# Performance work log

Hardware: AMD Instinct MI355X
Metric: run time of the kernel (lower is better)

## Reference

```python
import jax, jax.numpy as jnp
import numpy as np

EPS = 1e-5  # torch LayerNorm default


def _layer_norm(x, g, b):
    mu = jnp.mean(x, axis=-1, keepdims=True)
    var = jnp.mean(jnp.square(x - mu), axis=-1, keepdims=True)
    return (x - mu) * jax.lax.rsqrt(var + EPS) * g + b


def setup_inputs() -> dict:
    key = jax.random.key(0)
    ks = jax.random.split(key, 8)
    B, S, D = 4, 2048, 1024
    s = 1.0 / np.sqrt(D)
    return {
        "q": jax.random.normal(ks[0], (B, S, D), jnp.float32),
        "k": jax.random.normal(ks[1], (B, S, D), jnp.float32),
        "v": jax.random.normal(ks[2], (B, S, D), jnp.float32),
        "mask": jnp.ones((B, 1, S), jnp.int32),
        "Wq": jax.random.normal(ks[3], (D, D), jnp.float32) * s,
        "Wk": jax.random.normal(ks[4], (D, D), jnp.float32) * s,
        "Wv": jax.random.normal(ks[5], (D, D), jnp.float32) * s,
        "Wo": jax.random.normal(ks[6], (D, D), jnp.float32) * s,
        "ln_q_g": jnp.ones((D,), jnp.float32),
        "ln_q_b": jnp.zeros((D,), jnp.float32),
        "ln_k_g": jnp.ones((D,), jnp.float32),
        "ln_k_b": jnp.zeros((D,), jnp.float32),
        "ln_v_g": jnp.ones((D,), jnp.float32),
        "ln_v_b": jnp.zeros((D,), jnp.float32),
    }


def reference(q, k, v, mask, Wq, Wk, Wv, Wo,
              ln_q_g, ln_q_b, ln_k_g, ln_k_b, ln_v_g, ln_v_b):
    B, Lq, D = q.shape
    H = 16
    dk = D // H
    residual = q
    # pre-LN + bias-free projections
    qh = (_layer_norm(q, ln_q_g, ln_q_b) @ Wq).reshape(B, Lq, H, dk).transpose(0, 2, 1, 3)
    kh = (_layer_norm(k, ln_k_g, ln_k_b) @ Wk).reshape(B, -1, H, dk).transpose(0, 2, 1, 3)
    vh = (_layer_norm(v, ln_v_g, ln_v_b) @ Wv).reshape(B, -1, H, dk).transpose(0, 2, 1, 3)
    # scaled scores [B,H,Lq,Lk]
    scores = jnp.einsum('bhqd,bhkd->bhqk', qh, kh) / jnp.sqrt(jnp.float32(dk))
    pad = (mask == 0)[:, None, :, :]  # [B,1,*,Lk], True where masked
    scores = jnp.where(pad, -jnp.inf, scores)
    attn = jax.nn.softmax(scores, axis=-1)
    attn = jnp.where(pad, 0.0, attn)
    out = jnp.einsum('bhqk,bhkd->bhqd', attn, vh)
    out = out.transpose(0, 2, 1, 3).reshape(B, Lq, D)
    return out @ Wo + residual
```

## Files before the change

### kernel.cpp

```cpp
#include <hip/hip_runtime.h>
#include <stdint.h>

typedef __attribute__((ext_vector_type(8))) short short8;
typedef __attribute__((ext_vector_type(4))) float f32x4;
typedef __attribute__((ext_vector_type(4))) unsigned short us4;

#define B_ 4
#define S_ 2048
#define D_ 1024
#define H_ 16
#define DK_ 64

__device__ __forceinline__ unsigned short f2bf(float f) {
  union { float f; unsigned int u; } c; c.f = f;
  unsigned int r = (c.u + 0x7fffu + ((c.u >> 16) & 1u)) >> 16;
  return (unsigned short)r;
}

__device__ __forceinline__ unsigned int cvt_pk_bf16(float lo, float hi) {
  unsigned int r;
  asm("v_cvt_pk_bf16_f32 %0, %1, %2" : "=v"(r) : "v"(lo), "v"(hi));
  return r;
}

__device__ __forceinline__ float exp2_fast(float x) {
#if __has_builtin(__builtin_amdgcn_exp2f)
  return __builtin_amdgcn_exp2f(x);
#else
  float r; asm("v_exp_f32 %0, %1" : "=v"(r) : "v"(x)); return r;
#endif
}

__device__ __forceinline__ void glds16(const void* g, void* l) {
  __builtin_amdgcn_global_load_lds(
      (__attribute__((address_space(1))) void*)(uintptr_t)g,
      (__attribute__((address_space(3))) void*)l, 16, 0, 0);
}

__device__ __forceinline__ f32x4 mfma_bf16(short8 a, short8 b, f32x4 c) {
  return __builtin_amdgcn_mfma_f32_16x16x32_bf16(a, b, c, 0, 0, 0);
}

__global__ __launch_bounds__(256) void ln_bf16_3(const float* __restrict__ x0,
                                                 const float* __restrict__ x1,
                                                 const float* __restrict__ x2,
                                                 const float* __restrict__ g0,
                                                 const float* __restrict__ g1,
                                                 const float* __restrict__ g2,
                                                 const float* __restrict__ b0,
                                                 const float* __restrict__ b1,
                                                 const float* __restrict__ b2,
                                                 unsigned short* __restrict__ y0,
                                                 unsigned short* __restrict__ y1,
                                                 unsigned short* __restrict__ y2) {
  const int which = blockIdx.y;
  const float* x = which == 0 ? x0 : (which == 1 ? x1 : x2);
  const float* g = which == 0 ? g0 : (which == 1 ? g1 : g2);
  const float* bta = which == 0 ? b0 : (which == 1 ? b1 : b2);
  unsigned short* y = which == 0 ? y0 : (which == 1 ? y1 : y2);

  const int lane = threadIdx.x & 63, wid = threadIdx.x >> 6;
  const int row = blockIdx.x * 4 + wid;
  const float4* xr = (const float4*)(x + (size_t)row * D_);
  float4 v[4];
  float s1 = 0.f, s2 = 0.f;
#pragma unroll
  for (int i = 0; i < 4; ++i) {
    v[i] = xr[i * 64 + lane];
    s1 += v[i].x + v[i].y + v[i].z + v[i].w;
    s2 += v[i].x * v[i].x + v[i].y * v[i].y + v[i].z * v[i].z + v[i].w * v[i].w;
  }
#pragma unroll
  for (int m = 32; m; m >>= 1) { s1 += __shfl_xor(s1, m); s2 += __shfl_xor(s2, m); }
  const float mu = s1 * (1.f / D_);
  const float inv = rsqrtf(s2 * (1.f / D_) - mu * mu + 1e-5f);
  const float4* gp = (const float4*)g;
  const float4* bp = (const float4*)bta;
  us4* yr = (us4*)(y + (size_t)row * D_);
#pragma unroll
  for (int i = 0; i < 4; ++i) {
    float4 gv = gp[i * 64 + lane], bv = bp[i * 64 + lane];
    us4 o;
    o[0] = f2bf((v[i].x - mu) * inv * gv.x + bv.x);
    o[1] = f2bf((v[i].y - mu) * inv * gv.y + bv.y);
    o[2] = f2bf((v[i].z - mu) * inv * gv.z + bv.z);
    o[3] = f2bf((v[i].w - mu) * inv * gv.w + bv.w);
    yr[i * 64 + lane] = o;
  }
}

__global__ void wt_bf16_4(const float* __restrict__ W0, const float* __restrict__ W1,
                          const float* __restrict__ W2, const float* __restrict__ W3,
                          unsigned short* __restrict__ T0, unsigned short* __restrict__ T1,
                          unsigned short* __restrict__ T2, unsigned short* __restrict__ T3) {
  const int which = blockIdx.z;
  const float* W = which == 0 ? W0 : (which == 1 ? W1 : (which == 2 ? W2 : W3));
  unsigned short* Wt = which == 0 ? T0 : (which == 1 ? T1 : (which == 2 ? T2 : T3));
  __shared__ float t[32][33];
  const int n0 = blockIdx.x * 32, k0 = blockIdx.y * 32;
  const int tx = threadIdx.x, ty = threadIdx.y;
  for (int i = ty; i < 32; i += 8) t[i][tx] = W[(size_t)(k0 + i) * D_ + n0 + tx];
  __syncthreads();
  for (int i = ty; i < 32; i += 8)
    Wt[(size_t)(n0 + i) * D_ + k0 + tx] = f2bf(t[tx][i]);
}

template <int MODE>
__global__ __launch_bounds__(256, 2) void gemm_bt(const unsigned short* __restrict__ A,
                                                  const unsigned short* __restrict__ Bt,
                                                  void* __restrict__ outp, float scale,
                                                  const float* __restrict__ resid) {
  constexpr int K = D_;
  constexpr int NT = K / 64;
  __shared__ __attribute__((aligned(16))) unsigned short As[2][128][64];
  __shared__ __attribute__((aligned(16))) unsigned short Bs[2][128][64];
  const int tid = threadIdx.x;
  const int lane = tid & 63, wid = tid >> 6;
  const int lo16 = lane & 15, hi4 = lane >> 4;
  const int wr = wid >> 1, wc = wid & 1;
  const int gx = (int)gridDim.x;
  const int lid = (int)blockIdx.x + gx * (int)blockIdx.y;
  const int nwg = gx * (int)gridDim.y;
  const int swid = (lid & 7) * (nwg >> 3) + (lid >> 3);
  const int mbase = (swid / gx) * 128, nbase = (swid % gx) * 128;
  const int srow = lane >> 3, scol = (lane & 7) * 8;

  f32x4 acc[4][4] = {};

  auto stage = [&](int bufi, int kt) {
    const int kb = kt * 64;
#pragma unroll
    for (int c = 0; c < 4; ++c) {
      const int ch = wid * 4 + c;
      glds16(A + (size_t)(mbase + ch * 8 + srow) * K + kb + scol,
             (unsigned short*)&As[bufi][0][0] + ch * 512);
      glds16(Bt + (size_t)(nbase + ch * 8 + srow) * K + kb + scol,
             (unsigned short*)&Bs[bufi][0][0] + ch * 512);
    }
  };

  stage(0, 0);
  int cur = 0;

  for (int kt = 0; kt < NT; ++kt) {
    __syncthreads();
    if (kt + 1 < NT) stage(cur ^ 1, kt + 1);
    const unsigned short* Ap = &As[cur][0][0];
    const unsigned short* Bp = &Bs[cur][0][0];
    __builtin_amdgcn_s_setprio(1);
#pragma unroll
    for (int kk = 0; kk < 2; ++kk) {
      short8 af[4], bfr[4];
#pragma unroll
      for (int i = 0; i < 4; ++i)
        af[i] = *(const short8*)(Ap + (wr * 64 + i * 16 + lo16) * 64 + kk * 32 + hi4 * 8);
#pragma unroll
      for (int j = 0; j < 4; ++j)
        bfr[j] = *(const short8*)(Bp + (wc * 64 + j * 16 + lo16) * 64 + kk * 32 + hi4 * 8);
#pragma unroll
      for (int i = 0; i < 4; ++i)
#pragma unroll
        for (int j = 0; j < 4; ++j) acc[i][j] = mfma_bf16(af[i], bfr[j], acc[i][j]);
    }
    __builtin_amdgcn_s_setprio(0);
    cur ^= 1;
  }

  if (MODE == 0) {
    unsigned short* out = (unsigned short*)outp;
#pragma unroll
    for (int i = 0; i < 4; ++i) {
      const int row = mbase + wr * 64 + i * 16 + hi4 * 4;
      const int b = row >> 11, s = row & (S_ - 1);
#pragma unroll
      for (int j = 0; j < 4; ++j) {
        const int col = nbase + wc * 64 + j * 16 + lo16;
        const int h = col >> 6, d = col & 63;
        const size_t base = ((size_t)(b * H_ + h) * S_ + s) * DK_ + d;
#pragma unroll
        for (int r = 0; r < 4; ++r) out[base + (size_t)r * DK_] = f2bf(acc[i][j][r] * scale);
      }
    }
  } else if (MODE == 1) {
    float* out = (float*)outp;
#pragma unroll
    for (int i = 0; i < 4; ++i) {
      const int row = mbase + wr * 64 + i * 16 + hi4 * 4;
#pragma unroll
      for (int j = 0; j < 4; ++j) {
        const int col = nbase + wc * 64 + j * 16 + lo16;
        const size_t idx = (size_t)row * D_ + col;
#pragma unroll
        for (int r = 0; r < 4; ++r)
          out[idx + (size_t)r * D_] = acc[i][j][r] + resid[idx + (size_t)r * D_];
      }
    }
  } else {
    unsigned short* out = (unsigned short*)outp;
#pragma unroll
    for (int i = 0; i < 4; ++i) {
      const int row = mbase + wr * 64 + i * 16 + hi4 * 4;
      const int b = row >> 11, s0 = row & (S_ - 1);
#pragma unroll
      for (int j = 0; j < 4; ++j) {
        const int col = nbase + wc * 64 + j * 16 + lo16;
        const int h = col >> 6, d = col & 63;
        us4 w;
#pragma unroll
        for (int r = 0; r < 4; ++r) w[r] = f2bf(acc[i][j][r]);
        *(us4*)(out + ((size_t)(b * H_ + h) * DK_ + d) * S_ + s0) = w;
      }
    }
  }
}

__global__ __launch_bounds__(512, 2) void attn_k(const unsigned short* __restrict__ Qh,
                                                 const unsigned short* __restrict__ Kh,
                                                 const unsigned short* __restrict__ Vt,
                                                 const int* __restrict__ mask,
                                                 unsigned short* __restrict__ O) {
  __shared__ __attribute__((aligned(16))) unsigned short Ks[2][64][64];
  __shared__ __attribute__((aligned(16))) unsigned short Vs[2][64][64];
  __shared__ __attribute__((aligned(16))) unsigned short Ps[256][64];
  __shared__ unsigned short MskL[S_];
  __shared__ unsigned char TileOk[S_ / 64];
  const int tid = threadIdx.x, lane = tid & 63, wid = tid >> 6;
  const int lo16 = lane & 15, hi4 = lane >> 4;
  const int swz = (lo16 & 7) << 3;
  const int lid = (int)blockIdx.x + 8 * (int)blockIdx.y;
  const int swid = (lid & 7) * 64 + (lid >> 3);
  const int qb = swid & 7, bh = swid >> 3;
  const int b = bh >> 4, h = bh & 15;
  const unsigned short* Qb = Qh + (size_t)bh * S_ * DK_;
  const unsigned short* Kb = Kh + (size_t)bh * S_ * DK_;
  const unsigned short* Vb = Vt + (size_t)bh * DK_ * S_;
  const int* mb = mask + b * S_;
  const int srow = lane >> 3;
  const int scolx = ((lane & 7) ^ srow) * 8;

  for (int t = tid; t < S_; t += 512) MskL[t] = (unsigned short)(mb[t] != 0);
  __syncthreads();
  if (tid < S_ / 64) {
    int ok = 1;
    for (int j = 0; j < 64; ++j) ok &= (int)MskL[tid * 64 + j];
    TileOk[tid] = (unsigned char)ok;
  }

  short8 qf[2][2];
#pragma unroll
  for (int i = 0; i < 2; ++i)
#pragma unroll
    for (int kk = 0; kk < 2; ++kk)
      qf[i][kk] = *(const short8*)(Qb + (size_t)(qb * 256 + wid * 32 + i * 16 + lo16) * DK_ +
                                   kk * 32 + hi4 * 8);

  f32x4 o[2][4] = {};
  float lsum0 = 0.f, lsum1 = 0.f;

  auto stageKV = [&](int bufi, int kt) {
    glds16(Kb + (size_t)(kt * 64 + wid * 8 + srow) * DK_ + scolx,
           (unsigned short*)&Ks[bufi][0][0] + wid * 512);
    glds16(Vb + (size_t)(wid * 8 + srow) * S_ + kt * 64 + scolx,
           (unsigned short*)&Vs[bufi][0][0] + wid * 512);
  };

  stageKV(0, 0);
  int cur = 0;

  for (int kt = 0; kt < S_ / 64; ++kt) {
    __syncthreads();
    if (kt + 1 < S_ / 64) stageKV(cur ^ 1, kt + 1);

    const unsigned short* Kc = &Ks[cur][0][0];
    const int tok = (int)TileOk[kt];
#pragma unroll
    for (int i = 0; i < 2; ++i) {
      f32x4 p[4] = {};
      __builtin_amdgcn_s_setprio(1);
#pragma unroll
      for (int kk = 0; kk < 2; ++kk)
#pragma unroll
        for (int nf = 0; nf < 4; ++nf) {
          short8 kf = *(const short8*)(Kc + (nf * 16 + lo16) * 64 + ((kk * 32 + hi4 * 8) ^ swz));
          p[nf] = mfma_bf16(kf, qf[i][kk], p[nf]);
        }
      __builtin_amdgcn_s_setprio(0);
      if (!tok) {
#pragma unroll
        for (int nf = 0; nf < 4; ++nf) {
          const us4 mk = *(const us4*)&MskL[kt * 64 + nf * 16 + hi4 * 4];
#pragma unroll
          for (int r = 0; r < 4; ++r)
            if (!mk[r]) p[nf][r] = -1e30f;
        }
      }
      const int prow = wid * 32 + i * 16 + lo16;
      float ls = 0.f;
#pragma unroll
      for (int nf = 0; nf < 4; ++nf) {
        float e0 = exp2_fast(p[nf][0]);
        float e1 = exp2_fast(p[nf][1]);
        float e2 = exp2_fast(p[nf][2]);
        float e3 = exp2_fast(p[nf][3]);
        ls += (e0 + e1) + (e2 + e3);
        uint2 w;
        w.x = cvt_pk_bf16(e0, e1);
        w.y = cvt_pk_bf16(e2, e3);
        *(uint2*)&Ps[prow][(nf * 16 + hi4 * 4) ^ swz] = w;
      }
      if (i == 0) lsum0 += ls; else lsum1 += ls;
    }
    asm volatile("s_waitcnt lgkmcnt(0)" ::: "memory");
    __builtin_amdgcn_sched_barrier(0);
    const unsigned short* Vc = &Vs[cur][0][0];
    __builtin_amdgcn_s_setprio(1);
#pragma unroll
    for (int kk = 0; kk < 2; ++kk) {
      const int pc = (kk * 32 + hi4 * 8) ^ swz;
      short8 pa0 = *(const short8*)((const unsigned short*)Ps + (wid * 32 + 0 + lo16) * 64 + pc);
      short8 pa1 = *(const short8*)((const unsigned short*)Ps + (wid * 32 + 16 + lo16) * 64 + pc);
#pragma unroll
      for (int df = 0; df < 4; ++df) {
        short8 vf = *(const short8*)(Vc + (df * 16 + lo16) * 64 + pc);
        o[0][df] = mfma_bf16(pa0, vf, o[0][df]);
        o[1][df] = mfma_bf16(pa1, vf, o[1][df]);
      }
    }
    __builtin_amdgcn_s_setprio(0);
    cur ^= 1;
  }

  lsum0 += __shfl_xor(lsum0, 16); lsum0 += __shfl_xor(lsum0, 32);
  lsum1 += __shfl_xor(lsum1, 16); lsum1 += __shfl_xor(lsum1, 32);
#pragma unroll
  for (int i = 0; i < 2; ++i) {
#pragma unroll
    for (int r = 0; r < 4; ++r) {
      const int ql = hi4 * 4 + r;
      const float l = __shfl(i == 0 ? lsum0 : lsum1, ql);
      const float rl = l > 0.f ? 1.f / l : 0.f;
      const int srowg = qb * 256 + wid * 32 + i * 16 + ql;
      const size_t base = ((size_t)b * S_ + srowg) * D_ + h * 64;
#pragma unroll
      for (int df = 0; df < 4; ++df) O[base + df * 16 + lo16] = f2bf(o[i][df][r] * rl);
    }
  }
}

extern "C" void kernel_launch(void* const* d_in, const int* in_sizes, int n_in,
                              void* d_out, int out_size, void* d_ws, size_t ws_size,
                              hipStream_t stream) {
  const float* q = (const float*)d_in[0];
  const float* k = (const float*)d_in[1];
  const float* v = (const float*)d_in[2];
  const int* mask = (const int*)d_in[3];
  const float* Wq = (const float*)d_in[4];
  const float* Wk = (const float*)d_in[5];
  const float* Wv = (const float*)d_in[6];
  const float* Wo = (const float*)d_in[7];
  const float* lnqg = (const float*)d_in[8];
  const float* lnqb = (const float*)d_in[9];
  const float* lnkg = (const float*)d_in[10];
  const float* lnkb = (const float*)d_in[11];
  const float* lnvg = (const float*)d_in[12];
  const float* lnvb = (const float*)d_in[13];

  uint8_t* ws = (uint8_t*)d_ws;
  const size_t MB = 1024ull * 1024ull;
  unsigned short* Xq = (unsigned short*)(ws + 0 * MB);
  unsigned short* Xk = (unsigned short*)(ws + 16 * MB);
  unsigned short* Xv = (unsigned short*)(ws + 32 * MB);
  unsigned short* Wqt = (unsigned short*)(ws + 48 * MB);
  unsigned short* Wkt = (unsigned short*)(ws + 50 * MB);
  unsigned short* Wvt = (unsigned short*)(ws + 52 * MB);
  unsigned short* Wot = (unsigned short*)(ws + 54 * MB);
  unsigned short* Qh = (unsigned short*)(ws + 56 * MB);
  unsigned short* Kh = (unsigned short*)(ws + 72 * MB);
  unsigned short* Vtb = Xq;
  unsigned short* Ob = Xk;

  hipLaunchKernelGGL(wt_bf16_4, dim3(32, 32, 4), dim3(32, 8), 0, stream,
                     Wq, Wk, Wv, Wo, Wqt, Wkt, Wvt, Wot);

  hipLaunchKernelGGL(ln_bf16_3, dim3(2048, 3), dim3(256), 0, stream,
                     q, k, v, lnqg, lnkg, lnvg, lnqb, lnkb, lnvb, Xq, Xk, Xv);

  dim3 gg(D_ / 128, (B_ * S_) / 128);
  const float qscale = 0.125f * 1.4426950408889634f;
  hipLaunchKernelGGL(gemm_bt<0>, gg, dim3(256), 0, stream, Xq, Wqt, (void*)Qh, qscale, (const float*)nullptr);
  hipLaunchKernelGGL(gemm_bt<0>, gg, dim3(256), 0, stream, Xk, Wkt, (void*)Kh, 1.0f, (const float*)nullptr);
  hipLaunchKernelGGL(gemm_bt<2>, gg, dim3(256), 0, stream, Xv, Wvt, (void*)Vtb, 1.0f, (const float*)nullptr);

  hipLaunchKernelGGL(attn_k, dim3(S_ / 256, B_ * H_), dim3(512), 0, stream, Qh, Kh, Vtb, mask, Ob);

  hipLaunchKernelGGL(gemm_bt<1>, gg, dim3(256), 0, stream, Ob, Wot, d_out, 1.0f, q);
}
```

Before: 225.1 us.

## Batch QKV GEMMs into one launch and restructure attention tile loop

The three Q/K/V projection GEMMs become a single launch using blockIdx.z to pick inputs, outputs and epilogue. This removes two launches and lets the projection blocks fill the GPU together. The attention kernel now preloads K fragments before the QK MFMAs and pads the P buffer to 72 columns in place of the XOR swizzle. It also unrolls the KV loop by two with fixed buffer indices and drops the explicit lgkmcnt wait and sched barrier. The padding uses more shared memory, and dropping the wait relies on the compiler to order the LDS accesses correctly.

```diff
diff --git a/kernel.cpp b/kernel.cpp
--- a/kernel.cpp
+++ b/kernel.cpp
@@ -105,11 +105,113 @@
     Wt[(size_t)(n0 + i) * D_ + k0 + tx] = f2bf(t[tx][i]);
 }
 
-template <int MODE>
-__global__ __launch_bounds__(256, 2) void gemm_bt(const unsigned short* __restrict__ A,
-                                                  const unsigned short* __restrict__ Bt,
-                                                  void* __restrict__ outp, float scale,
-                                                  const float* __restrict__ resid) {
+__global__ __launch_bounds__(256, 2) void gemm_qkv(const unsigned short* __restrict__ Xq,
+                                                   const unsigned short* __restrict__ Xk,
+                                                   const unsigned short* __restrict__ Xv,
+                                                   const unsigned short* __restrict__ Wq,
+                                                   const unsigned short* __restrict__ Wk,
+                                                   const unsigned short* __restrict__ Wv,
+                                                   unsigned short* __restrict__ Qh,
+                                                   unsigned short* __restrict__ Kh,
+                                                   unsigned short* __restrict__ Vtb,
+                                                   float qscale) {
+  constexpr int K = D_;
+  constexpr int NT = K / 64;
+  __shared__ __attribute__((aligned(16))) unsigned short As[2][128][64];
+  __shared__ __attribute__((aligned(16))) unsigned short Bs[2][128][64];
+  const int z = blockIdx.z;
+  const unsigned short* A = z == 0 ? Xq : (z == 1 ? Xk : Xv);
+  const unsigned short* Bt = z == 0 ? Wq : (z == 1 ? Wk : Wv);
+  const int tid = threadIdx.x;
+  const int lane = tid & 63, wid = tid >> 6;
+  const int lo16 = lane & 15, hi4 = lane >> 4;
+  const int wr = wid >> 1, wc = wid & 1;
+  const int gx = (int)gridDim.x;
+  const int lid = (int)blockIdx.x + gx * (int)blockIdx.y;
+  const int nwg = gx * (int)gridDim.y;
+  const int swid = (lid & 7) * (nwg >> 3) + (lid >> 3);
+  const int mbase = (swid / gx) * 128, nbase = (swid % gx) * 128;
+  const int srow = lane >> 3, scol = (lane & 7) * 8;
+
+  f32x4 acc[4][4] = {};
+
+  auto stage = [&](int bufi, int kt) {
+    const int kb = kt * 64;
+#pragma unroll
+    for (int c = 0; c < 4; ++c) {
+      const int ch = wid * 4 + c;
+      glds16(A + (size_t)(mbase + ch * 8 + srow) * K + kb + scol,
+             (unsigned short*)&As[bufi][0][0] + ch * 512);
+      glds16(Bt + (size_t)(nbase + ch * 8 + srow) * K + kb + scol,
+             (unsigned short*)&Bs[bufi][0][0] + ch * 512);
+    }
+  };
+
+  stage(0, 0);
+  int cur = 0;
+
+  for (int kt = 0; kt < NT; ++kt) {
+    __syncthreads();
+    if (kt + 1 < NT) stage(cur ^ 1, kt + 1);
+    const unsigned short* Ap = &As[cur][0][0];
+    const unsigned short* Bp = &Bs[cur][0][0];
+    __builtin_amdgcn_s_setprio(1);
+#pragma unroll
+    for (int kk = 0; kk < 2; ++kk) {
+      short8 af[4], bfr[4];
+#pragma unroll
+      for (int i = 0; i < 4; ++i)
+        af[i] = *(const short8*)(Ap + (wr * 64 + i * 16 + lo16) * 64 + kk * 32 + hi4 * 8);
+#pragma unroll
+      for (int j = 0; j < 4; ++j)
+        bfr[j] = *(const short8*)(Bp + (wc * 64 + j * 16 + lo16) * 64 + kk * 32 + hi4 * 8);
+#pragma unroll
+      for (int i = 0; i < 4; ++i)
+#pragma unroll
+        for (int j = 0; j < 4; ++j) acc[i][j] = mfma_bf16(af[i], bfr[j], acc[i][j]);
+    }
+    __builtin_amdgcn_s_setprio(0);
+    cur ^= 1;
+  }
+
+  if (z < 2) {
+    unsigned short* out = z == 0 ? Qh : Kh;
+    const float scale = z == 0 ? qscale : 1.0f;
+#pragma unroll
+    for (int i = 0; i < 4; ++i) {
+      const int row = mbase + wr * 64 + i * 16 + hi4 * 4;
+      const int b = row >> 11, s = row & (S_ - 1);
+#pragma unroll
+      for (int j = 0; j < 4; ++j) {
+        const int col = nbase + wc * 64 + j * 16 + lo16;
+        const int h = col >> 6, d = col & 63;
+        const size_t base = ((size_t)(b * H_ + h) * S_ + s) * DK_ + d;
+#pragma unroll
+        for (int r = 0; r < 4; ++r) out[base + (size_t)r * DK_] = f2bf(acc[i][j][r] * scale);
+      }
+    }
+  } else {
+#pragma unroll
+    for (int i = 0; i < 4; ++i) {
+      const int row = mbase + wr * 64 + i * 16 + hi4 * 4;
+      const int b = row >> 11, s0 = row & (S_ - 1);
+#pragma unroll
+      for (int j = 0; j < 4; ++j) {
+        const int col = nbase + wc * 64 + j * 16 + lo16;
+        const int h = col >> 6, d = col & 63;
+        us4 w;
+#pragma unroll
+        for (int r = 0; r < 4; ++r) w[r] = f2bf(acc[i][j][r]);
+        *(us4*)(Vtb + ((size_t)(b * H_ + h) * DK_ + d) * S_ + s0) = w;
+      }
+    }
+  }
+}
+
+__global__ __launch_bounds__(256, 2) void gemm_out(const unsigned short* __restrict__ A,
+                                                   const unsigned short* __restrict__ Bt,
+                                                   float* __restrict__ out,
+                                                   const float* __restrict__ resid) {
   constexpr int K = D_;
   constexpr int NT = K / 64;
   __shared__ __attribute__((aligned(16))) unsigned short As[2][128][64];
@@ -166,50 +268,16 @@
     cur ^= 1;
   }
 
-  if (MODE == 0) {
-    unsigned short* out = (unsigned short*)outp;
-#pragma unroll
-    for (int i = 0; i < 4; ++i) {
-      const int row = mbase + wr * 64 + i * 16 + hi4 * 4;
-      const int b = row >> 11, s = row & (S_ - 1);
-#pragma unroll
-      for (int j = 0; j < 4; ++j) {
-        const int col = nbase + wc * 64 + j * 16 + lo16;
-        const int h = col >> 6, d = col & 63;
-        const size_t base = ((size_t)(b * H_ + h) * S_ + s) * DK_ + d;
-#pragma unroll
-        for (int r = 0; r < 4; ++r) out[base + (size_t)r * DK_] = f2bf(acc[i][j][r] * scale);
-      }
-    }
-  } else if (MODE == 1) {
-    float* out = (float*)outp;
-#pragma unroll
-    for (int i = 0; i < 4; ++i) {
-      const int row = mbase + wr * 64 + i * 16 + hi4 * 4;
-#pragma unroll
-      for (int j = 0; j < 4; ++j) {
-        const int col = nbase + wc * 64 + j * 16 + lo16;
-        const size_t idx = (size_t)row * D_ + col;
-#pragma unroll
-        for (int r = 0; r < 4; ++r)
-          out[idx + (size_t)r * D_] = acc[i][j][r] + resid[idx + (size_t)r * D_];
-      }
-    }
-  } else {
-    unsigned short* out = (unsigned short*)outp;
-#pragma unroll
-    for (int i = 0; i < 4; ++i) {
-      const int row = mbase + wr * 64 + i * 16 + hi4 * 4;
-      const int b = row >> 11, s0 = row & (S_ - 1);
-#pragma unroll
-      for (int j = 0; j < 4; ++j) {
-        const int col = nbase + wc * 64 + j * 16 + lo16;
-        const int h = col >> 6, d = col & 63;
-        us4 w;
-#pragma unroll
-        for (int r = 0; r < 4; ++r) w[r] = f2bf(acc[i][j][r]);
-        *(us4*)(out + ((size_t)(b * H_ + h) * DK_ + d) * S_ + s0) = w;
-      }
+#pragma unroll
+  for (int i = 0; i < 4; ++i) {
+    const int row = mbase + wr * 64 + i * 16 + hi4 * 4;
+#pragma unroll
+    for (int j = 0; j < 4; ++j) {
+      const int col = nbase + wc * 64 + j * 16 + lo16;
+      const size_t idx = (size_t)row * D_ + col;
+#pragma unroll
+      for (int r = 0; r < 4; ++r)
+        out[idx + (size_t)r * D_] = acc[i][j][r] + resid[idx + (size_t)r * D_];
     }
   }
 }
@@ -221,7 +289,7 @@
                                                  unsigned short* __restrict__ O) {
   __shared__ __attribute__((aligned(16))) unsigned short Ks[2][64][64];
   __shared__ __attribute__((aligned(16))) unsigned short Vs[2][64][64];
-  __shared__ __attribute__((aligned(16))) unsigned short Ps[256][64];
+  __shared__ __attribute__((aligned(16))) unsigned short Ps[256][72];
   __shared__ unsigned short MskL[S_];
   __shared__ unsigned char TileOk[S_ / 64];
   const int tid = threadIdx.x, lane = tid & 63, wid = tid >> 6;
@@ -264,15 +332,18 @@
            (unsigned short*)&Vs[bufi][0][0] + wid * 512);
   };
 
-  stageKV(0, 0);
-  int cur = 0;
-
-  for (int kt = 0; kt < S_ / 64; ++kt) {
+  auto tile = [&](int bufc, int kt) {
     __syncthreads();
-    if (kt + 1 < S_ / 64) stageKV(cur ^ 1, kt + 1);
-
-    const unsigned short* Kc = &Ks[cur][0][0];
+    if (kt + 1 < S_ / 64) stageKV(bufc ^ 1, kt + 1);
+
+    const unsigned short* Kc = &Ks[bufc][0][0];
     const int tok = (int)TileOk[kt];
+    short8 kf[2][4];
+#pragma unroll
+    for (int kk = 0; kk < 2; ++kk)
+#pragma unroll
+      for (int nf = 0; nf < 4; ++nf)
+        kf[kk][nf] = *(const short8*)(Kc + (nf * 16 + lo16) * 64 + ((kk * 32 + hi4 * 8) ^ swz));
 #pragma unroll
     for (int i = 0; i < 2; ++i) {
       f32x4 p[4] = {};
@@ -280,10 +351,7 @@
 #pragma unroll
       for (int kk = 0; kk < 2; ++kk)
 #pragma unroll
-        for (int nf = 0; nf < 4; ++nf) {
-          short8 kf = *(const short8*)(Kc + (nf * 16 + lo16) * 64 + ((kk * 32 + hi4 * 8) ^ swz));
-          p[nf] = mfma_bf16(kf, qf[i][kk], p[nf]);
-        }
+        for (int nf = 0; nf < 4; ++nf) p[nf] = mfma_bf16(kf[kk][nf], qf[i][kk], p[nf]);
       __builtin_amdgcn_s_setprio(0);
       if (!tok) {
 #pragma unroll
@@ -306,28 +374,32 @@
         uint2 w;
         w.x = cvt_pk_bf16(e0, e1);
         w.y = cvt_pk_bf16(e2, e3);
-        *(uint2*)&Ps[prow][(nf * 16 + hi4 * 4) ^ swz] = w;
+        *(uint2*)&Ps[prow][nf * 16 + hi4 * 4] = w;
       }
       if (i == 0) lsum0 += ls; else lsum1 += ls;
     }
-    asm volatile("s_waitcnt lgkmcnt(0)" ::: "memory");
-    __builtin_amdgcn_sched_barrier(0);
-    const unsigned short* Vc = &Vs[cur][0][0];
+    const unsigned short* Vc = &Vs[bufc][0][0];
     __builtin_amdgcn_s_setprio(1);
 #pragma unroll
     for (int kk = 0; kk < 2; ++kk) {
-      const int pc = (kk * 32 + hi4 * 8) ^ swz;
-      short8 pa0 = *(const short8*)((const unsigned short*)Ps + (wid * 32 + 0 + lo16) * 64 + pc);
-      short8 pa1 = *(const short8*)((const unsigned short*)Ps + (wid * 32 + 16 + lo16) * 64 + pc);
+      const int pc = kk * 32 + hi4 * 8;
+      short8 pa0 = *(const short8*)&Ps[wid * 32 + 0 + lo16][pc];
+      short8 pa1 = *(const short8*)&Ps[wid * 32 + 16 + lo16][pc];
 #pragma unroll
       for (int df = 0; df < 4; ++df) {
-        short8 vf = *(const short8*)(Vc + (df * 16 + lo16) * 64 + pc);
+        short8 vf = *(const short8*)(Vc + (df * 16 + lo16) * 64 + (pc ^ swz));
         o[0][df] = mfma_bf16(pa0, vf, o[0][df]);
         o[1][df] = mfma_bf16(pa1, vf, o[1][df]);
       }
     }
     __builtin_amdgcn_s_setprio(0);
-    cur ^= 1;
+  };
+
+  stageKV(0, 0);
+#pragma unroll 1
+  for (int kt = 0; kt < S_ / 64; kt += 2) {
+    tile(0, kt);
+    tile(1, kt + 1);
   }
 
   lsum0 += __shfl_xor(lsum0, 16); lsum0 += __shfl_xor(lsum0, 32);
@@ -385,13 +457,12 @@
   hipLaunchKernelGGL(ln_bf16_3, dim3(2048, 3), dim3(256), 0, stream,
                      q, k, v, lnqg, lnkg, lnvg, lnqb, lnkb, lnvb, Xq, Xk, Xv);
 
-  dim3 gg(D_ / 128, (B_ * S_) / 128);
   const float qscale = 0.125f * 1.4426950408889634f;
-  hipLaunchKernelGGL(gemm_bt<0>, gg, dim3(256), 0, stream, Xq, Wqt, (void*)Qh, qscale, (const float*)nullptr);
-  hipLaunchKernelGGL(gemm_bt<0>, gg, dim3(256), 0, stream, Xk, Wkt, (void*)Kh, 1.0f, (const float*)nullptr);
-  hipLaunchKernelGGL(gemm_bt<2>, gg, dim3(256), 0, stream, Xv, Wvt, (void*)Vtb, 1.0f, (const float*)nullptr);
+  hipLaunchKernelGGL(gemm_qkv, dim3(D_ / 128, (B_ * S_) / 128, 3), dim3(256), 0, stream,
+                     Xq, Xk, Xv, Wqt, Wkt, Wvt, Qh, Kh, Vtb, qscale);
 
   hipLaunchKernelGGL(attn_k, dim3(S_ / 256, B_ * H_), dim3(512), 0, stream, Qh, Kh, Vtb, mask, Ob);
 
-  hipLaunchKernelGGL(gemm_bt<1>, gg, dim3(256), 0, stream, Ob, Wot, d_out, 1.0f, q);
-}
+  hipLaunchKernelGGL(gemm_out, dim3(D_ / 128, (B_ * S_) / 128), dim3(256), 0, stream,
+                     Ob, Wot, (float*)d_out, q);
+}
```

Measured after the change: 237.6 us. 5.5% more time.
